# Kernel optimization log

Measured on AMD Instinct MI355X. Metric: run time of the kernel, lower is better.

Reference implementation:

```python
import jax, jax.numpy as jnp
import numpy as np

D_MODEL = 1024
N_HEADS = 16
D_K = D_MODEL // N_HEADS


def setup_inputs() -> dict:
    key = jax.random.key(0)
    k1, k2, k3 = jax.random.split(key, 3)
    x = jax.random.normal(k1, (4, 2048, D_MODEL), dtype=jnp.float32)
    # torch nn.Linear(d, 3d, bias=False): y = x @ W.T ; we store W.T directly as (in, out)
    w_qkv = jax.random.normal(k2, (D_MODEL, 3 * D_MODEL), dtype=jnp.float32) * (1.0 / np.sqrt(D_MODEL))
    w_out = jax.random.normal(k3, (D_MODEL, D_MODEL), dtype=jnp.float32) * (1.0 / np.sqrt(D_MODEL))
    return {"x": x, "w_qkv": w_qkv, "w_out": w_out}


def reference(x, w_qkv, w_out):
    B, T, D = x.shape
    qkv = jnp.einsum('btd,de->bte', x, w_qkv)  # (B,T,3D)
    q, k, v = jnp.split(qkv, 3, axis=-1)
    # split heads -> (B,H,T,d_k)
    def split_heads(t):
        return t.reshape(B, T, N_HEADS, D_K).transpose(0, 2, 1, 3)
    q, k, v = split_heads(q), split_heads(k), split_heads(v)
    scale = 1.0 / np.sqrt(D_K).astype(np.float32)
    scores = jnp.einsum('bhqd,bhkd->bhqk', q, k) * scale  # (B,H,T,T)
    causal = jnp.triu(jnp.full((T, T), -jnp.inf, dtype=scores.dtype), k=1)
    scores = scores + causal[None, None]
    weights = jax.nn.softmax(scores, axis=-1)
    attn = jnp.einsum('bhqk,bhkd->bhqd', weights, v)
    attn = attn.transpose(0, 2, 1, 3).reshape(B, T, D)
    return jnp.einsum('btd,de->bte', attn, w_out)
```

## Files before the change

kernel.cpp:

```cpp
#include <hip/hip_runtime.h>
#include <hip/hip_bf16.h>

typedef short short8 __attribute__((ext_vector_type(8)));
typedef float f32x4 __attribute__((ext_vector_type(4)));
typedef float f32x16 __attribute__((ext_vector_type(16)));

#define MFMA16(a, b, c) __builtin_amdgcn_mfma_f32_16x16x32_bf16((a), (b), (c), 0, 0, 0)
#define MFMA32(a, b, c) __builtin_amdgcn_mfma_f32_32x32x16_bf16((a), (b), (c), 0, 0, 0)

#define GLOAD16(gp, lp)                                                    \
    __builtin_amdgcn_global_load_lds(                                      \
        (const __attribute__((address_space(1))) unsigned int*)(gp),       \
        (__attribute__((address_space(3))) unsigned int*)(lp), 16, 0, 0)

__device__ __forceinline__ unsigned short f2b(float x) {
    unsigned int u = __float_as_uint(x);
    unsigned int r = u + 0x7FFFu + ((u >> 16) & 1u);
    return (unsigned short)(r >> 16);
}

#if __has_builtin(__builtin_amdgcn_cvt_pk_bf16_f32)
__device__ __forceinline__ unsigned pack2(float a, float b) {
    auto v = __builtin_amdgcn_cvt_pk_bf16_f32(a, b);
    unsigned u;
    __builtin_memcpy(&u, &v, 4);
    return u;
}
#else
__device__ __forceinline__ unsigned pack2(float a, float b) {
    return (unsigned)f2b(a) | ((unsigned)f2b(b) << 16);
}
#endif

__global__ __launch_bounds__(256) void cast4_kernel(const float* __restrict__ in,
                                                    unsigned short* __restrict__ out,
                                                    int n4) {
    int i = blockIdx.x * 256 + threadIdx.x;
    if (i < n4) {
        float4 v = ((const float4*)in)[i];
        ushort4 o;
        o.x = f2b(v.x); o.y = f2b(v.y); o.z = f2b(v.z); o.w = f2b(v.w);
        ((ushort4*)out)[i] = o;
    }
}

__global__ __launch_bounds__(256) void transpose_cast_f32(const float* __restrict__ in,
                                                          unsigned short* __restrict__ out,
                                                          int K, int N) {
    __shared__ unsigned short Ls[64 * 66];
    const int k0 = blockIdx.y * 64, n0 = blockIdx.x * 64;
    const int tid = threadIdx.x;
    const int krow = tid >> 4, nc4 = (tid & 15) * 4;
#pragma unroll
    for (int p = 0; p < 4; p++) {
        float4 v = *(const float4*)(in + (size_t)(k0 + krow + p * 16) * N + n0 + nc4);
        unsigned* d32 = (unsigned*)(Ls + (krow + p * 16) * 66 + nc4);
        d32[0] = pack2(v.x, v.y);
        d32[1] = pack2(v.z, v.w);
    }
    __syncthreads();
    const int n = tid >> 3, kc = (tid & 7) * 8;
#pragma unroll
    for (int p = 0; p < 2; p++) {
        int nn = n + p * 32;
        unsigned short w[8];
#pragma unroll
        for (int j = 0; j < 8; j++) w[j] = Ls[(kc + j) * 66 + nn];
        *(short8*)(out + (size_t)(n0 + nn) * K + k0 + kc) = *(short8*)w;
    }
}

__global__ __launch_bounds__(512, 2) void gemm_qkv(const unsigned short* __restrict__ A,
                                                   const unsigned short* __restrict__ Bt,
                                                   unsigned short* __restrict__ Qb,
                                                   unsigned short* __restrict__ Kb,
                                                   unsigned short* __restrict__ Vt) {
    __shared__ __align__(16) unsigned short smem[65536];

    const int tid  = threadIdx.x;
    const int wave = tid >> 6;
    const int lane = tid & 63;
    const int l32  = lane & 31;
    const int hi   = lane >> 5;
    const int wr   = wave >> 2;
    const int wc   = wave & 3;

    const int bid = blockIdx.x;
    const int sid = (bid & 7) * 48 + (bid >> 3);
    const int bx  = sid % 12;
    const int by  = sid / 12;
    const int m0 = by * 256;
    const int n0 = bx * 256;

    const int srow = tid >> 3;
    const int cswz = (((tid & 7) ^ ((tid >> 3) & 7)) * 8);
    const unsigned short* gA = A  + (size_t)(m0 + srow) * 1024 + cswz;
    const unsigned short* gB = Bt + (size_t)(n0 + srow) * 1024 + cswz;

#define STAGE_A(buf, h, kt) do {                                              \
        const unsigned short* _g = gA + (size_t)((h) * 128) * 1024 + (kt) * 64; \
        unsigned short* _l = smem + (buf) * 16384 + (h) * 8192 + wave * 512;  \
        GLOAD16(_g, _l);                                                      \
        GLOAD16(_g + 65536, _l + 4096);                                       \
    } while (0)
#define STAGE_B(buf, h, kt) do {                                              \
        const unsigned short* _g = gB + (size_t)((h) * 128) * 1024 + (kt) * 64; \
        unsigned short* _l = smem + 32768 + (buf) * 16384 + (h) * 8192 + wave * 512; \
        GLOAD16(_g, _l);                                                      \
        GLOAD16(_g + 65536, _l + 4096);                                       \
    } while (0)

    const int sw7  = l32 & 7;
    const int aoff = (wr * 128 + l32) * 64;
    const int boff = (wc * 64 + l32) * 64;

    f32x16 acc[4][2] = {};

    STAGE_A(0, 0, 0); STAGE_A(0, 1, 0); STAGE_B(0, 0, 0); STAGE_B(0, 1, 0);
    STAGE_B(1, 0, 1); STAGE_B(1, 1, 1); STAGE_A(1, 0, 1);
    asm volatile("s_waitcnt vmcnt(6)" ::: "memory");
    __builtin_amdgcn_s_barrier();

#pragma unroll
    for (int t = 0; t < 16; ++t) {
        const int b = t & 1;
        const unsigned short* Ab = smem + b * 16384;
        const unsigned short* Bb = smem + 32768 + b * 16384;

        short8 afLo[2][4], afHi[2][4], bf0[4], bf1[4];

#pragma unroll
        for (int rf = 0; rf < 2; ++rf)
#pragma unroll
            for (int ks = 0; ks < 4; ++ks)
                afLo[rf][ks] = *(const short8*)(Ab + aoff + rf * 2048 + (((ks * 2 + hi) ^ sw7) * 8));
#pragma unroll
        for (int ks = 0; ks < 4; ++ks)
            bf0[ks] = *(const short8*)(Bb + boff + (((ks * 2 + hi) ^ sw7) * 8));
        if (t + 1 < 16) STAGE_A(b ^ 1, 1, t + 1);
        __builtin_amdgcn_s_barrier();
        asm volatile("s_waitcnt lgkmcnt(0)" ::: "memory");
        __builtin_amdgcn_s_setprio(1);
#pragma unroll
        for (int ks = 0; ks < 4; ++ks) {
            acc[0][0] = MFMA32(afLo[0][ks], bf0[ks], acc[0][0]);
            acc[1][0] = MFMA32(afLo[1][ks], bf0[ks], acc[1][0]);
        }
        __builtin_amdgcn_s_setprio(0);
        __builtin_amdgcn_s_barrier();

#pragma unroll
        for (int ks = 0; ks < 4; ++ks)
            bf1[ks] = *(const short8*)(Bb + boff + 2048 + (((ks * 2 + hi) ^ sw7) * 8));
        __builtin_amdgcn_s_barrier();
        asm volatile("s_waitcnt lgkmcnt(0)" ::: "memory");
        __builtin_amdgcn_s_setprio(1);
#pragma unroll
        for (int ks = 0; ks < 4; ++ks) {
            acc[0][1] = MFMA32(afLo[0][ks], bf1[ks], acc[0][1]);
            acc[1][1] = MFMA32(afLo[1][ks], bf1[ks], acc[1][1]);
        }
        __builtin_amdgcn_s_setprio(0);
        __builtin_amdgcn_s_barrier();

#pragma unroll
        for (int rf = 0; rf < 2; ++rf)
#pragma unroll
            for (int ks = 0; ks < 4; ++ks)
                afHi[rf][ks] = *(const short8*)(Ab + aoff + (2 + rf) * 2048 + (((ks * 2 + hi) ^ sw7) * 8));
        if (t + 2 < 16) { STAGE_B(b, 0, t + 2); STAGE_B(b, 1, t + 2); }
        __builtin_amdgcn_s_barrier();
        asm volatile("s_waitcnt lgkmcnt(0)" ::: "memory");
        __builtin_amdgcn_s_setprio(1);
#pragma unroll
        for (int ks = 0; ks < 4; ++ks) {
            acc[2][0] = MFMA32(afHi[0][ks], bf0[ks], acc[2][0]);
            acc[3][0] = MFMA32(afHi[1][ks], bf0[ks], acc[3][0]);
        }
        __builtin_amdgcn_s_setprio(0);
        __builtin_amdgcn_s_barrier();

        if (t + 2 < 16) {
            STAGE_A(b, 0, t + 2);
            asm volatile("s_waitcnt vmcnt(6)" ::: "memory");
        } else {
            asm volatile("s_waitcnt vmcnt(0)" ::: "memory");
        }
        __builtin_amdgcn_s_barrier();
        __builtin_amdgcn_s_setprio(1);
#pragma unroll
        for (int ks = 0; ks < 4; ++ks) {
            acc[2][1] = MFMA32(afHi[0][ks], bf1[ks], acc[2][1]);
            acc[3][1] = MFMA32(afHi[1][ks], bf1[ks], acc[3][1]);
        }
        __builtin_amdgcn_s_setprio(0);
        __builtin_amdgcn_s_barrier();
    }
#undef STAGE_A
#undef STAGE_B

    if (n0 < 2048) {
        unsigned short* outp = (n0 < 1024) ? Qb : Kb;
        const int cb = (n0 < 1024) ? n0 : n0 - 1024;
        const float QS = (n0 < 1024) ? 0.125f * 1.44269504f : 1.0f;
#pragma unroll
        for (int rf = 0; rf < 4; ++rf)
#pragma unroll
            for (int cf = 0; cf < 2; ++cf)
#pragma unroll
                for (int r = 0; r < 16; ++r) {
                    int row = m0 + wr * 128 + rf * 32 + (r & 3) + 8 * (r >> 2) + 4 * hi;
                    int col = cb + wc * 64 + cf * 32 + l32;
                    outp[(size_t)row * 1024 + col] = f2b(acc[rf][cf][r] * QS);
                }
    } else {
        const int bb = m0 >> 11, t0b = m0 & 2047;
        const int hbase = (n0 - 2048) >> 6;
        unsigned short* reg = smem + wc * 16384;
#pragma unroll
        for (int rf = 0; rf < 4; ++rf)
#pragma unroll
            for (int cf = 0; cf < 2; ++cf)
#pragma unroll
                for (int rg = 0; rg < 4; ++rg) {
                    const int tl = wr * 128 + rf * 32 + rg * 8 + 4 * hi;
                    const int d  = cf * 32 + l32;
                    const int w  = d * 128 + ((tl >> 1) ^ (4 * (d & 7)));
                    uint2 v;
                    v.x = pack2(acc[rf][cf][4 * rg + 0], acc[rf][cf][4 * rg + 1]);
                    v.y = pack2(acc[rf][cf][4 * rg + 2], acc[rf][cf][4 * rg + 3]);
                    *(uint2*)(reg + 2 * w) = v;
                }
        __syncthreads();
#pragma unroll
        for (int it = 0; it < 16; ++it) {
            const int id = it * 512 + tid;
            const int hh = id >> 11, d = (id >> 5) & 63, k = id & 31;
            short8 v = *(const short8*)(smem + hh * 16384 +
                                        2 * (d * 128 + ((4 * k) ^ (4 * (d & 7)))));
            *(short8*)(Vt + ((size_t)((bb * 16 + hbase + hh) * 64 + d)) * 2048 + t0b + k * 8) = v;
        }
    }
}

__global__ __launch_bounds__(256) void gemm_out(const unsigned short* __restrict__ A,
                                                const unsigned short* __restrict__ Bt,
                                                float* __restrict__ C) {
    const int K = 1024, lda = 1024;
    __shared__ unsigned short As[64 * 32];
    __shared__ unsigned short Bs[128 * 32];

    const int tid  = threadIdx.x;
    const int wave = tid >> 6;
    const int lane = tid & 63;
    const int l32  = lane & 31;
    const int hi   = lane >> 5;
    const int m0 = blockIdx.y * 64;
    const int n0 = blockIdx.x * 128;
    const int wm = (wave >> 1) * 32;
    const int wn = (wave & 1) * 64;

    const int srow = lane >> 2;
    const int scol = (((lane & 3) ^ ((lane >> 3) & 3)) * 8);
    const int fsw  = ((l32 >> 1) & 3);

    const unsigned short* Ag  = A  + (size_t)(m0 + wave * 16 + srow) * lda + scol;
    const unsigned short* Bg0 = Bt + (size_t)(n0 + wave * 32 + srow)      * K + scol;
    const unsigned short* Bg1 = Bt + (size_t)(n0 + wave * 32 + 16 + srow) * K + scol;
    unsigned short* Al  = As + wave * 512;
    unsigned short* Bl0 = Bs + (wave * 2 + 0) * 512;
    unsigned short* Bl1 = Bs + (wave * 2 + 1) * 512;

    f32x16 acc[2] = {};

    for (int k0 = 0; k0 < K; k0 += 32) {
        __syncthreads();
        GLOAD16(Ag + k0, Al);
        GLOAD16(Bg0 + k0, Bl0);
        GLOAD16(Bg1 + k0, Bl1);
        __syncthreads();

        short8 af[2], bf[2][2];
        {
            const int row = wm + l32;
#pragma unroll
            for (int ks = 0; ks < 2; ks++)
                af[ks] = *(const short8*)(As + row * 32 + ((ks * 2 + hi) ^ fsw) * 8);
        }
#pragma unroll
        for (int j = 0; j < 2; j++) {
            const int row = wn + j * 32 + l32;
#pragma unroll
            for (int ks = 0; ks < 2; ks++)
                bf[j][ks] = *(const short8*)(Bs + row * 32 + ((ks * 2 + hi) ^ fsw) * 8);
        }
#pragma unroll
        for (int ks = 0; ks < 2; ks++)
#pragma unroll
            for (int j = 0; j < 2; j++)
                acc[j] = MFMA32(af[ks], bf[j][ks], acc[j]);
    }

#pragma unroll
    for (int j = 0; j < 2; j++)
#pragma unroll
        for (int r = 0; r < 16; r++) {
            int row = m0 + wm + (r & 3) + 8 * (r >> 2) + 4 * hi;
            int col = n0 + wn + j * 32 + l32;
            C[(size_t)row * 1024 + col] = acc[j][r];
        }
}

__global__ __launch_bounds__(256) void attention_kernel(const unsigned short* Qb,
                                                        const unsigned short* Kb,
                                                        const unsigned short* Vt,
                                                        unsigned short* attn) {
    const int T = 2048;
    const int bi = blockIdx.x;
    const int qb = 31 - (bi >> 6);
    const int hb = bi & 63;
    const int b = hb >> 4, h = hb & 15;
    const int qb0 = qb * 64;
    const int tid = threadIdx.x, wave = tid >> 6, lane = tid & 63;
    const int l16 = lane & 15, quad = lane >> 4;
    const int qw0 = qb0 + wave * 16;

    const unsigned short* Qp  = Qb + (size_t)b * T * 1024 + h * 64;
    const unsigned short* Kp  = Kb + (size_t)b * T * 1024 + h * 64;
    const unsigned short* Vbh = Vt + ((size_t)(b * 16 + h) * 64) * 2048;

    __shared__ unsigned short Ks[2][64 * 32];
    __shared__ unsigned short Vts[2][64 * 32];
    __shared__ unsigned short Ps[4][16 * 40];
    unsigned short* Psw = Ps[wave];

    short8 qf[2];
#pragma unroll
    for (int kd = 0; kd < 2; kd++)
        qf[kd] = *(const short8*)(Qp + (size_t)(qw0 + l16) * 1024 + kd * 32 + quad * 8);

    f32x4 o[4] = {};
    float l_acc = 0.f;

    const int srow = lane >> 2;
    const int scol = (((lane & 3) ^ ((lane >> 3) & 3)) * 8);
    const int sw8  = ((l16 >> 1) & 3) * 8;
    const size_t ktstep = (wave < 2) ? (size_t)64 * 1024 : (size_t)64;
    const size_t cstep  = (wave < 2) ? (size_t)16 * 1024 : (size_t)16 * T;
    const unsigned short* g0 = (wave < 2)
            ? Kp + (size_t)srow * 1024 + wave * 32 + scol
            : Vbh + (size_t)srow * T + (wave - 2) * 32 + scol;
    unsigned short* l0 = (wave < 2) ? Ks[wave] : Vts[wave - 2];

    for (int kt = 0; kt <= qb; kt++) {
        const int tk0 = kt * 64;
        const unsigned short* g = g0 + (size_t)kt * ktstep;
        __syncthreads();
#pragma unroll
        for (int c = 0; c < 4; c++) GLOAD16(g + c * cstep, l0 + c * 512);
        __syncthreads();

#pragma unroll
        for (int th = 0; th < 2; th++) {
            if (tk0 + th * 32 > qw0 + 15) continue;

            f32x4 s[2];
            bool act[2];
#pragma unroll
            for (int mi = 0; mi < 2; mi++) {
                const int t0 = tk0 + (th * 2 + mi) * 16;
                act[mi] = (t0 <= qw0 + 15);
                s[mi] = (f32x4){0.f, 0.f, 0.f, 0.f};
                if (act[mi]) {
                    const int row = (th * 2 + mi) * 16 + l16;
                    short8 kf0 = *(const short8*)(Ks[0] + row * 32 + (quad * 8 ^ sw8));
                    short8 kf1 = *(const short8*)(Ks[1] + row * 32 + (quad * 8 ^ sw8));
                    s[mi] = MFMA16(kf0, qf[0], s[mi]);
                    s[mi] = MFMA16(kf1, qf[1], s[mi]);
                }
            }
#pragma unroll
            for (int mi = 0; mi < 2; mi++) {
                const int t0 = tk0 + (th * 2 + mi) * 16;
                unsigned pk0 = 0, pk1 = 0;
                if (act[mi]) {
                    const bool full = (t0 + 15) <= qw0;
                    float p[4];
#pragma unroll
                    for (int r = 0; r < 4; r++) {
                        float e = __builtin_amdgcn_exp2f(s[mi][r]);
                        if (!full)
                            e = (t0 + quad * 4 + r <= qw0 + l16) ? e : 0.f;
                        p[r] = e;
                    }
                    l_acc += (p[0] + p[1]) + (p[2] + p[3]);
                    pk0 = pack2(p[0], p[1]);
                    pk1 = pack2(p[2], p[3]);
                }
                uint2 pr; pr.x = pk0; pr.y = pk1;
                *(uint2*)(Psw + l16 * 40 + mi * 16 + quad * 4) = pr;
            }
            short8 pf = *(const short8*)(Psw + l16 * 40 + quad * 8);
#pragma unroll
            for (int dt = 0; dt < 4; dt++) {
                short8 vf = *(const short8*)(Vts[th] + (dt * 16 + l16) * 32 + (quad * 8 ^ sw8));
                o[dt] = MFMA16(vf, pf, o[dt]);
            }
        }
    }

    float l = l_acc;
    l += __shfl_xor(l, 16);
    l += __shfl_xor(l, 32);
    const float rl = 1.f / l;
    const int q = qw0 + l16;
#pragma unroll
    for (int dt = 0; dt < 4; dt++) {
        ushort4 wv;
        wv.x = f2b(o[dt][0] * rl);
        wv.y = f2b(o[dt][1] * rl);
        wv.z = f2b(o[dt][2] * rl);
        wv.w = f2b(o[dt][3] * rl);
        *(ushort4*)(attn + (size_t)(b * T + q) * 1024 + h * 64 + dt * 16 + quad * 4) = wv;
    }
}

extern "C" void kernel_launch(void* const* d_in, const int* in_sizes, int n_in,
                              void* d_out, int out_size, void* d_ws, size_t ws_size,
                              hipStream_t stream) {
    const float* x     = (const float*)d_in[0];
    const float* w_qkv = (const float*)d_in[1];
    const float* w_out = (const float*)d_in[2];
    float* out = (float*)d_out;

    const int M = 8192, D = 1024, E = 3072;
    const size_t MB = 1048576;

    char* ws = (char*)d_ws;
    unsigned short* xb    = (unsigned short*)ws;
    unsigned short* wqkvT = (unsigned short*)(ws + 16 * MB);
    unsigned short* woutT = (unsigned short*)(ws + 22 * MB);
    unsigned short* Qb    = (unsigned short*)(ws + 24 * MB);
    unsigned short* Kb    = (unsigned short*)(ws + 40 * MB);
    unsigned short* Vt    = (unsigned short*)(ws + 56 * MB);

    cast4_kernel<<<M * D / 4 / 256, 256, 0, stream>>>(x, xb, M * D / 4);
    transpose_cast_f32<<<dim3(E / 64, D / 64), 256, 0, stream>>>(w_qkv, wqkvT, D, E);
    transpose_cast_f32<<<dim3(D / 64, D / 64), 256, 0, stream>>>(w_out, woutT, D, D);

    gemm_qkv<<<dim3(384), 512, 0, stream>>>(xb, wqkvT, Qb, Kb, Vt);

    attention_kernel<<<dim3(2048), 256, 0, stream>>>(Qb, Kb, Vt, Qb);

    gemm_out<<<dim3(D / 128, M / 64), 256, 0, stream>>>(Qb, woutT, out);
}
```

Baseline: 257.3 us.

## Keep attention probabilities in registers via permuted V-transpose layout and MFMA row-sum

```diff
diff --git a/kernel.cpp b/kernel.cpp
--- a/kernel.cpp
+++ b/kernel.cpp
@@ -236,8 +236,13 @@
         for (int it = 0; it < 16; ++it) {
             const int id = it * 512 + tid;
             const int hh = id >> 11, d = (id >> 5) & 63, k = id & 31;
-            short8 v = *(const short8*)(smem + hh * 16384 +
-                                        2 * (d * 128 + ((4 * k) ^ (4 * (d & 7)))));
+            const int kb = k >> 2, kl = k & 3;
+            const int xx = 4 * (d & 7);
+            const unsigned short* bp = smem + hh * 16384 + 2 * (d * 128);
+            uint2 lo  = *(const uint2*)(bp + 2 * ((16 * kb + 2 * kl) ^ xx));
+            uint2 hi2 = *(const uint2*)(bp + 2 * ((16 * kb + 2 * kl + 8) ^ xx));
+            uint2 parts[2] = {lo, hi2};
+            short8 v; __builtin_memcpy(&v, parts, 16);
             *(short8*)(Vt + ((size_t)((bb * 16 + hbase + hh) * 64 + d)) * 2048 + t0b + k * 8) = v;
         }
     }
@@ -331,8 +336,6 @@
 
     __shared__ unsigned short Ks[2][64 * 32];
     __shared__ unsigned short Vts[2][64 * 32];
-    __shared__ unsigned short Ps[4][16 * 40];
-    unsigned short* Psw = Ps[wave];
 
     short8 qf[2];
 #pragma unroll
@@ -340,7 +343,12 @@
         qf[kd] = *(const short8*)(Qp + (size_t)(qw0 + l16) * 1024 + kd * 32 + quad * 8);
 
     f32x4 o[4] = {};
-    float l_acc = 0.f;
+    f32x4 o_l = {};
+    const f32x4 fz = {};
+
+    short8 onesf;
+#pragma unroll
+    for (int e = 0; e < 8; e++) onesf[e] = (short)0x3F80;
 
     const int srow = lane >> 2;
     const int scol = (((lane & 3) ^ ((lane >> 3) & 3)) * 8);
@@ -362,45 +370,61 @@
 
 #pragma unroll
         for (int th = 0; th < 2; th++) {
-            if (tk0 + th * 32 > qw0 + 15) continue;
-
-            f32x4 s[2];
-            bool act[2];
-#pragma unroll
-            for (int mi = 0; mi < 2; mi++) {
-                const int t0 = tk0 + (th * 2 + mi) * 16;
-                act[mi] = (t0 <= qw0 + 15);
-                s[mi] = (f32x4){0.f, 0.f, 0.f, 0.f};
-                if (act[mi]) {
-                    const int row = (th * 2 + mi) * 16 + l16;
-                    short8 kf0 = *(const short8*)(Ks[0] + row * 32 + (quad * 8 ^ sw8));
-                    short8 kf1 = *(const short8*)(Ks[1] + row * 32 + (quad * 8 ^ sw8));
-                    s[mi] = MFMA16(kf0, qf[0], s[mi]);
-                    s[mi] = MFMA16(kf1, qf[1], s[mi]);
+            const int t0a = tk0 + th * 64 / 2;
+            if (t0a > qw0 + 15) continue;
+            const int t1 = t0a + 16;
+            const bool act1 = (t1 <= qw0 + 15);
+
+            f32x4 s0, s1;
+            {
+                const int row = (th * 2) * 16 + l16;
+                short8 kf0 = *(const short8*)(Ks[0] + row * 32 + (quad * 8 ^ sw8));
+                short8 kf1 = *(const short8*)(Ks[1] + row * 32 + (quad * 8 ^ sw8));
+                s0 = MFMA16(kf0, qf[0], fz);
+                s0 = MFMA16(kf1, qf[1], s0);
+            }
+            if (act1) {
+                const int row = (th * 2 + 1) * 16 + l16;
+                short8 kf0 = *(const short8*)(Ks[0] + row * 32 + (quad * 8 ^ sw8));
+                short8 kf1 = *(const short8*)(Ks[1] + row * 32 + (quad * 8 ^ sw8));
+                s1 = MFMA16(kf0, qf[0], fz);
+                s1 = MFMA16(kf1, qf[1], s1);
+            }
+
+            unsigned u00, u01, u10, u11;
+            {
+                const bool full = (t0a + 15) <= qw0;
+                float p[4];
+#pragma unroll
+                for (int r = 0; r < 4; r++) {
+                    float e = __builtin_amdgcn_exp2f(s0[r]);
+                    if (!full)
+                        e = (t0a + quad * 4 + r <= qw0 + l16) ? e : 0.f;
+                    p[r] = e;
                 }
+                u00 = pack2(p[0], p[1]);
+                u01 = pack2(p[2], p[3]);
             }
-#pragma unroll
-            for (int mi = 0; mi < 2; mi++) {
-                const int t0 = tk0 + (th * 2 + mi) * 16;
-                unsigned pk0 = 0, pk1 = 0;
-                if (act[mi]) {
-                    const bool full = (t0 + 15) <= qw0;
-                    float p[4];
-#pragma unroll
-                    for (int r = 0; r < 4; r++) {
-                        float e = __builtin_amdgcn_exp2f(s[mi][r]);
-                        if (!full)
-                            e = (t0 + quad * 4 + r <= qw0 + l16) ? e : 0.f;
-                        p[r] = e;
-                    }
-                    l_acc += (p[0] + p[1]) + (p[2] + p[3]);
-                    pk0 = pack2(p[0], p[1]);
-                    pk1 = pack2(p[2], p[3]);
+            if (act1) {
+                const bool full = (t1 + 15) <= qw0;
+                float p[4];
+#pragma unroll
+                for (int r = 0; r < 4; r++) {
+                    float e = __builtin_amdgcn_exp2f(s1[r]);
+                    if (!full)
+                        e = (t1 + quad * 4 + r <= qw0 + l16) ? e : 0.f;
+                    p[r] = e;
                 }
-                uint2 pr; pr.x = pk0; pr.y = pk1;
-                *(uint2*)(Psw + l16 * 40 + mi * 16 + quad * 4) = pr;
+                u10 = pack2(p[0], p[1]);
+                u11 = pack2(p[2], p[3]);
+            } else {
+                u10 = 0; u11 = 0;
             }
-            short8 pf = *(const short8*)(Psw + l16 * 40 + quad * 8);
+
+            unsigned pb[4] = {u00, u01, u10, u11};
+            short8 pf; __builtin_memcpy(&pf, pb, 16);
+
+            o_l = MFMA16(onesf, pf, o_l);
 #pragma unroll
             for (int dt = 0; dt < 4; dt++) {
                 short8 vf = *(const short8*)(Vts[th] + (dt * 16 + l16) * 32 + (quad * 8 ^ sw8));
@@ -409,10 +433,7 @@
         }
     }
 
-    float l = l_acc;
-    l += __shfl_xor(l, 16);
-    l += __shfl_xor(l, 32);
-    const float rl = 1.f / l;
+    const float rl = 1.f / o_l[0];
     const int q = qw0 + l16;
 #pragma unroll
     for (int dt = 0; dt < 4; dt++) {
```

Measured after the change: 255.9 us. Within noise of the previous version (-0.5%).
